# Performance work log

Measured on AMD Instinct MI355X. Metric: run time of the kernel, lower is better.

## Reference

```python
import jax, jax.numpy as jnp
import numpy as np

H, B, T, C = 1024, 256, 256, 10

def setup_inputs() -> dict:
    key = jax.random.key(0)
    ks = jax.random.split(key, 10)
    def xav(k, shape):
        fan_in, fan_out = shape[1], shape[0]
        lim = jnp.sqrt(6.0 / (fan_in + fan_out))
        return jax.random.uniform(k, shape, jnp.float32, -lim, lim)
    return {
        "x": jax.random.normal(ks[0], (B, T), jnp.float32),
        "W_gx": xav(ks[1], (H, 1)), "W_gh": xav(ks[2], (H, H)),
        "W_ix": xav(ks[3], (H, 1)), "W_ih": xav(ks[4], (H, H)),
        "W_fx": xav(ks[5], (H, 1)), "W_fh": xav(ks[6], (H, H)),
        "W_ox": xav(ks[7], (H, 1)), "W_oh": xav(ks[8], (H, H)),
        "W_ph": xav(ks[9], (C, H)),
        "b_g": jnp.zeros((B,), jnp.float32), "b_i": jnp.zeros((B,), jnp.float32),
        "b_f": jnp.zeros((B,), jnp.float32), "b_o": jnp.zeros((B,), jnp.float32),
        "b_p": jnp.zeros((B,), jnp.float32),
    }

def reference(x, W_gx, W_gh, W_ix, W_ih, W_fx, W_fh, W_ox, W_oh, W_ph,
              b_g, b_i, b_f, b_o, b_p):
    batch = x.shape[0]
    hidden = W_gh.shape[0]
    xs = x.T  # [T, B]; per-step x_t is a [1, B] row (input_dim = 1)

    def step(carry, x_t):
        h, c = carry                       # [H, B] each
        xr = x_t[None, :]                  # [1, B]
        g = jnp.tanh(W_gx @ xr + W_gh @ h + b_g)          # [H, B] + [B] broadcasts per column
        i = jax.nn.sigmoid(W_ix @ xr + W_ih @ h + b_i)
        f = jax.nn.sigmoid(W_fx @ xr + W_fh @ h + b_f)
        o = jax.nn.sigmoid(W_ox @ xr + W_oh @ h + b_o)
        c_new = g * i + c * f
        h_new = jnp.tanh(c_new) * o
        return (h_new, c_new), None

    h0 = jnp.zeros((hidden, batch), x.dtype)
    c0 = jnp.zeros((hidden, batch), x.dtype)
    (h_T, _), _ = jax.lax.scan(step, (h0, c0), xs)
    p = W_ph @ h_T + b_p                   # [C, B]
    y = jax.nn.softmax(p, axis=1)          # faithful: softmax over dim=1 (batch axis)
    return y.T                             # [B, C]
```

## Files before the change

### kernel.cpp

```cpp
#include <hip/hip_runtime.h>
#include <hip/hip_bf16.h>


#define H 1024
#define B 256
#define T 256
#define NCLS 10

typedef __attribute__((ext_vector_type(8))) short short8;
typedef __attribute__((ext_vector_type(4))) float f32x4;

__device__ inline unsigned short bf16_bits(float f) {
    union { __hip_bfloat16 h; unsigned short u; } cv;
    cv.h = __float2bfloat16(f);
    return cv.u;
}

#define L2E 1.4426950408889634f
__device__ inline float sigm_fast(float x) {
    float e = __builtin_amdgcn_exp2f(-L2E * x);
    return __builtin_amdgcn_rcpf(1.0f + e);
}
__device__ inline float tanh_fast(float x) {
    float e = __builtin_amdgcn_exp2f((2.0f * L2E) * x);
    return 1.0f - 2.0f * __builtin_amdgcn_rcpf(1.0f + e);
}


__global__ __launch_bounds__(512)
__attribute__((amdgpu_waves_per_eu(2, 2)))
void lstm_persist(
    const float* __restrict__ x,
    const float* __restrict__ Wgh, const float* __restrict__ Wih,
    const float* __restrict__ Wfh, const float* __restrict__ Woh,
    const float* __restrict__ Wgx, const float* __restrict__ Wix,
    const float* __restrict__ Wfx, const float* __restrict__ Wox,
    const float* __restrict__ bg, const float* __restrict__ bi,
    const float* __restrict__ bf_, const float* __restrict__ bo,
    char* __restrict__ frag,
    unsigned* __restrict__ flags,
    unsigned* __restrict__ det,
    float* __restrict__ hfin)
{
    __shared__ __align__(16) char hstage[65536];
    __shared__ float zb[2][4][32][36];
    __shared__ float wxl[4][32];
    __shared__ float bsl[4][32];
    __shared__ int sh_lcl;

    const int tid  = threadIdx.x;
    const int lane = tid & 63;
    const int wave = tid >> 6;
    const int gate = wave & 3;
    const int kh   = wave >> 2;
    const int bt = blockIdx.x & 7;
    const int jt = blockIdx.x >> 3;
    const int j0 = jt * 32;
    const int b0 = bt * 32;

    unsigned xcc;
    __asm__ volatile("s_getreg_b32 %0, hwreg(HW_REG_XCC_ID)" : "=s"(xcc));
    xcc &= 7u;
    if (tid == 0)
        __hip_atomic_store(&det[bt * 32 + jt], xcc + 1u,
                           __ATOMIC_RELAXED, __HIP_MEMORY_SCOPE_AGENT);

    if (tid < 128) {
        int g = tid >> 5, r = tid & 31;
        const float* wx = (g == 0) ? Wgx : (g == 1) ? Wix : (g == 2) ? Wfx : Wox;
        const float* bb = (g == 0) ? bg  : (g == 1) ? bi  : (g == 2) ? bf_ : bo;
        wxl[g][r] = wx[j0 + r];
        bsl[g][r] = bb[b0 + r];
    }

    const float* Wh = (gate == 0) ? Wgh : (gate == 1) ? Wih : (gate == 2) ? Wfh : Woh;
    short8 awreg[2][16];
#pragma unroll
    for (int mt = 0; mt < 2; ++mt) {
        const float* wrow = Wh + (j0 + 16 * mt + (lane & 15)) * H
                          + kh * 512 + ((lane >> 4) * 8);
#pragma unroll
        for (int c = 0; c < 16; ++c) {
            const float4 f0 = *(const float4*)(wrow + c * 32);
            const float4 f1 = *(const float4*)(wrow + c * 32 + 4);
            short8 s;
            s[0] = (short)bf16_bits(f0.x); s[1] = (short)bf16_bits(f0.y);
            s[2] = (short)bf16_bits(f0.z); s[3] = (short)bf16_bits(f0.w);
            s[4] = (short)bf16_bits(f1.x); s[5] = (short)bf16_bits(f1.y);
            s[6] = (short)bf16_bits(f1.z); s[7] = (short)bf16_bits(f1.w);
            awreg[mt][c] = s;
        }
    }
#pragma unroll
    for (int mt = 0; mt < 2; ++mt)
#pragma unroll
        for (int c = 0; c < 16; ++c)
            __asm__ volatile("" : "+a"(awreg[mt][c]));

    if (wave == 0) {
        unsigned v;
        while (true) {
            v = __hip_atomic_load(&det[bt * 32 + (lane & 31)],
                                  __ATOMIC_RELAXED, __HIP_MEMORY_SCOPE_AGENT);
            if (__all((int)(v != 0u))) break;
            __builtin_amdgcn_s_sleep(1);
        }
        int same = __all((int)(v == xcc + 1u));
        if (tid == 0) sh_lcl = same;
    }
    __syncthreads();
    const bool lcl = (sh_lcl != 0);

    float creg[2] = {0.f, 0.f};
    const int nn = tid & 31;
    const int aa = tid >> 5;

    unsigned* myflag = &flags[blockIdx.x * 32];
    unsigned* pollflag = &flags[(((unsigned)lane & 31) * 8 + bt) * 32];

    for (int t = 0; t < T; ++t) {
        const float xv = x[(b0 + nn) * T + t];

        if (wave == 0) {
            const unsigned target = (unsigned)t;
            while (true) {
                unsigned v = __hip_atomic_load(pollflag, __ATOMIC_RELAXED,
                                               __HIP_MEMORY_SCOPE_AGENT);
                if (__all((int)(v >= target))) break;
                __builtin_amdgcn_s_sleep(1);
            }
        }
        __syncthreads();

        f32x4 a00 = {0.f,0.f,0.f,0.f}, a01 = a00, a10 = a00, a11 = a00;

        if (t > 0) {
            {
                const char* gbase = frag + (t & 1) * 524288 + bt * 65536 + tid * 16;
                short8 v0, v1, v2, v3, v4, v5, v6, v7;
                if (lcl) {
                    __asm__ volatile(
                        "global_load_dwordx4 %0, %8, off sc0\n\t"
                        "global_load_dwordx4 %1, %9, off sc0\n\t"
                        "global_load_dwordx4 %2, %10, off sc0\n\t"
                        "global_load_dwordx4 %3, %11, off sc0\n\t"
                        "global_load_dwordx4 %4, %12, off sc0\n\t"
                        "global_load_dwordx4 %5, %13, off sc0\n\t"
                        "global_load_dwordx4 %6, %14, off sc0\n\t"
                        "global_load_dwordx4 %7, %15, off sc0\n\t"
                        "s_waitcnt vmcnt(0)"
                        : "=&v"(v0), "=&v"(v1), "=&v"(v2), "=&v"(v3),
                          "=&v"(v4), "=&v"(v5), "=&v"(v6), "=&v"(v7)
                        : "v"(gbase),         "v"(gbase + 8192),
                          "v"(gbase + 16384), "v"(gbase + 24576),
                          "v"(gbase + 32768), "v"(gbase + 40960),
                          "v"(gbase + 49152), "v"(gbase + 57344)
                        : "memory");
                } else {
                    __asm__ volatile(
                        "global_load_dwordx4 %0, %8, off sc0 sc1\n\t"
                        "global_load_dwordx4 %1, %9, off sc0 sc1\n\t"
                        "global_load_dwordx4 %2, %10, off sc0 sc1\n\t"
                        "global_load_dwordx4 %3, %11, off sc0 sc1\n\t"
                        "global_load_dwordx4 %4, %12, off sc0 sc1\n\t"
                        "global_load_dwordx4 %5, %13, off sc0 sc1\n\t"
                        "global_load_dwordx4 %6, %14, off sc0 sc1\n\t"
                        "global_load_dwordx4 %7, %15, off sc0 sc1\n\t"
                        "s_waitcnt vmcnt(0)"
                        : "=&v"(v0), "=&v"(v1), "=&v"(v2), "=&v"(v3),
                          "=&v"(v4), "=&v"(v5), "=&v"(v6), "=&v"(v7)
                        : "v"(gbase),         "v"(gbase + 8192),
                          "v"(gbase + 16384), "v"(gbase + 24576),
                          "v"(gbase + 32768), "v"(gbase + 40960),
                          "v"(gbase + 49152), "v"(gbase + 57344)
                        : "memory");
                }
                short8* dd = (short8*)hstage;
                dd[tid +    0] = v0;  dd[tid +  512] = v1;
                dd[tid + 1024] = v2;  dd[tid + 1536] = v3;
                dd[tid + 2048] = v4;  dd[tid + 2560] = v5;
                dd[tid + 3072] = v6;  dd[tid + 3584] = v7;
            }
            __syncthreads();

#pragma unroll
            for (int c = 0; c < 16; ++c) {
                const int cg = kh * 16 + c;
                short8 bf0 = *(const short8*)(hstage + cg * 1024 + lane * 16);
                short8 bf1 = *(const short8*)(hstage + 32768 + cg * 1024 + lane * 16);
                a00 = __builtin_amdgcn_mfma_f32_16x16x32_bf16(awreg[0][c], bf0, a00, 0, 0, 0);
                a01 = __builtin_amdgcn_mfma_f32_16x16x32_bf16(awreg[0][c], bf1, a01, 0, 0, 0);
                a10 = __builtin_amdgcn_mfma_f32_16x16x32_bf16(awreg[1][c], bf0, a10, 0, 0, 0);
                a11 = __builtin_amdgcn_mfma_f32_16x16x32_bf16(awreg[1][c], bf1, a11, 0, 0, 0);
            }
        }

        {
            const int cn = lane & 15;
            const int rb = (lane >> 4) * 4;
#pragma unroll
            for (int r = 0; r < 4; ++r) {
                zb[kh][gate][ 0 + rb + r][ 0 + cn] = a00[r];
                zb[kh][gate][ 0 + rb + r][16 + cn] = a01[r];
                zb[kh][gate][16 + rb + r][ 0 + cn] = a10[r];
                zb[kh][gate][16 + rb + r][16 + cn] = a11[r];
            }
        }
        __syncthreads();

        unsigned short hb[2];
#pragma unroll
        for (int q = 0; q < 2; ++q) {
            const int jl = 2 * aa + q;
            float zg = (zb[0][0][jl][nn] + zb[1][0][jl][nn]) + wxl[0][jl] * xv + bsl[0][nn];
            float zi = (zb[0][1][jl][nn] + zb[1][1][jl][nn]) + wxl[1][jl] * xv + bsl[1][nn];
            float zf = (zb[0][2][jl][nn] + zb[1][2][jl][nn]) + wxl[2][jl] * xv + bsl[2][nn];
            float zo = (zb[0][3][jl][nn] + zb[1][3][jl][nn]) + wxl[3][jl] * xv + bsl[3][nn];
            float g  = tanh_fast(zg);
            float ig = sigm_fast(zi);
            float fg = sigm_fast(zf);
            float og = sigm_fast(zo);
            creg[q] = g * ig + creg[q] * fg;
            float hn = tanh_fast(creg[q]) * og;
            hb[q] = bf16_bits(hn);
            if (t == T - 1) hfin[(j0 + jl) * B + (b0 + nn)] = hn;
        }
        {
            const unsigned val = (unsigned)hb[0] | ((unsigned)hb[1] << 16);
            short* fb = (short*)(frag + ((t + 1) & 1) * 524288);
            short* fdst = fb + ((2 * bt + (nn >> 4)) * 32 + jt) * 512
                        + ((aa >> 2) * 16 + (nn & 15)) * 8 + (aa & 3) * 2;
            if (lcl) {
                *(volatile unsigned*)fdst = val;
            } else {
                __hip_atomic_store((unsigned*)fdst, val, __ATOMIC_RELAXED,
                                   __HIP_MEMORY_SCOPE_AGENT);
            }
        }

        __syncthreads();
        if (tid == 0) {
            __asm__ volatile("s_waitcnt vmcnt(0)" ::: "memory");
            __hip_atomic_store(myflag, (unsigned)(t + 1), __ATOMIC_RELAXED,
                               __HIP_MEMORY_SCOPE_AGENT);
        }
    }
}

__global__ __launch_bounds__(256) void lstm_final(
    const float* __restrict__ Wph, const float* __restrict__ hfin,
    const float* __restrict__ bp, float* __restrict__ out)
{
    __shared__ float sh[256];
    __shared__ float shm, shs;
    int c = blockIdx.x;
    int b = threadIdx.x;
    float acc = bp[b];
    const float* wr = Wph + c * H;
    for (int k = 0; k < H; ++k)
        acc += wr[k] * hfin[k * B + b];

    sh[b] = acc;
    __syncthreads();
    for (int s = 128; s > 0; s >>= 1) {
        if (b < s) sh[b] = fmaxf(sh[b], sh[b + s]);
        __syncthreads();
    }
    if (b == 0) shm = sh[0];
    __syncthreads();
    float e = expf(acc - shm);
    sh[b] = e;
    __syncthreads();
    for (int s = 128; s > 0; s >>= 1) {
        if (b < s) sh[b] += sh[b + s];
        __syncthreads();
    }
    if (b == 0) shs = sh[0];
    __syncthreads();
    out[b * NCLS + c] = e / shs;
}

extern "C" void kernel_launch(void* const* d_in, const int* in_sizes, int n_in,
                              void* d_out, int out_size, void* d_ws, size_t ws_size,
                              hipStream_t stream)
{
    const float* x   = (const float*)d_in[0];
    const float* Wgx = (const float*)d_in[1];
    const float* Wgh = (const float*)d_in[2];
    const float* Wix = (const float*)d_in[3];
    const float* Wih = (const float*)d_in[4];
    const float* Wfx = (const float*)d_in[5];
    const float* Wfh = (const float*)d_in[6];
    const float* Wox = (const float*)d_in[7];
    const float* Woh = (const float*)d_in[8];
    const float* Wph = (const float*)d_in[9];
    const float* bg  = (const float*)d_in[10];
    const float* bi  = (const float*)d_in[11];
    const float* bfv = (const float*)d_in[12];
    const float* bo  = (const float*)d_in[13];
    const float* bp  = (const float*)d_in[14];

    char* ws = (char*)d_ws;
    char* frag = ws;
    unsigned* flags = (unsigned*)(ws + 1048576);
    unsigned* det   = (unsigned*)(ws + 1081344);
    float* hfin = (float*)(ws + 1085440);

    hipMemsetAsync(flags, 0, 36864, stream);

    lstm_persist<<<256, 512, 0, stream>>>(
        x, Wgh, Wih, Wfh, Woh, Wgx, Wix, Wfx, Wox,
        bg, bi, bfv, bo, frag, flags, det, hfin);

    lstm_final<<<NCLS, 256, 0, stream>>>(Wph, hfin, bp, (float*)d_out);
}
```

Before: 1.163 ms.

## Switch recurrent matmul to 32x32x16 MFMA with K split across four waves

Each wave now computes two gates over a 32x32 tile with 32x32x16 bf16 MFMAs, and the K dimension is split into quarters across four waves instead of halves. Partial sums are written to a swizzled LDS buffer and reduced by 256 threads, which each produce four hidden rows and store 64-bit packed bf16 fragments in a new layout. The aim is fewer MFMA issues and fewer B-fragment LDS reads per step. In exchange the LDS reduction grows to four partials, and half the threads sit idle during the elementwise phase.

```diff
diff --git a/kernel.cpp b/kernel.cpp
--- a/kernel.cpp
+++ b/kernel.cpp
@@ -9,6 +9,8 @@
 
 typedef __attribute__((ext_vector_type(8))) short short8;
 typedef __attribute__((ext_vector_type(4))) float f32x4;
+typedef __attribute__((ext_vector_type(16))) float f32x16;
+typedef unsigned long long ull;
 
 __device__ inline unsigned short bf16_bits(float f) {
     union { __hip_bfloat16 h; unsigned short u; } cv;
@@ -43,7 +45,7 @@
     float* __restrict__ hfin)
 {
     __shared__ __align__(16) char hstage[65536];
-    __shared__ float zb[2][4][32][36];
+    __shared__ __align__(16) float zb[16][32][32];
     __shared__ float wxl[4][32];
     __shared__ float bsl[4][32];
     __shared__ int sh_lcl;
@@ -51,8 +53,8 @@
     const int tid  = threadIdx.x;
     const int lane = tid & 63;
     const int wave = tid >> 6;
-    const int gate = wave & 3;
-    const int kh   = wave >> 2;
+    const int gp   = wave >> 2;
+    const int kq   = wave & 3;
     const int bt = blockIdx.x & 7;
     const int jt = blockIdx.x >> 3;
     const int j0 = jt * 32;
@@ -73,29 +75,31 @@
         bsl[g][r] = bb[b0 + r];
     }
 
-    const float* Wh = (gate == 0) ? Wgh : (gate == 1) ? Wih : (gate == 2) ? Wfh : Woh;
+    const float* Wlo = (gp == 0) ? Wgh : Wfh;
+    const float* Whi = (gp == 0) ? Wih : Woh;
     short8 awreg[2][16];
 #pragma unroll
-    for (int mt = 0; mt < 2; ++mt) {
-        const float* wrow = Wh + (j0 + 16 * mt + (lane & 15)) * H
-                          + kh * 512 + ((lane >> 4) * 8);
+    for (int gg = 0; gg < 2; ++gg) {
+        const float* Wp = gg ? Whi : Wlo;
+        const float* wrow = Wp + (j0 + (lane & 31)) * H
+                          + kq * 256 + ((lane >> 5) * 8);
 #pragma unroll
         for (int c = 0; c < 16; ++c) {
-            const float4 f0 = *(const float4*)(wrow + c * 32);
-            const float4 f1 = *(const float4*)(wrow + c * 32 + 4);
+            const float4 f0 = *(const float4*)(wrow + c * 16);
+            const float4 f1 = *(const float4*)(wrow + c * 16 + 4);
             short8 s;
             s[0] = (short)bf16_bits(f0.x); s[1] = (short)bf16_bits(f0.y);
             s[2] = (short)bf16_bits(f0.z); s[3] = (short)bf16_bits(f0.w);
             s[4] = (short)bf16_bits(f1.x); s[5] = (short)bf16_bits(f1.y);
             s[6] = (short)bf16_bits(f1.z); s[7] = (short)bf16_bits(f1.w);
-            awreg[mt][c] = s;
-        }
-    }
-#pragma unroll
-    for (int mt = 0; mt < 2; ++mt)
+            awreg[gg][c] = s;
+        }
+    }
+#pragma unroll
+    for (int gg = 0; gg < 2; ++gg)
 #pragma unroll
         for (int c = 0; c < 16; ++c)
-            __asm__ volatile("" : "+a"(awreg[mt][c]));
+            __asm__ volatile("" : "+a"(awreg[gg][c]));
 
     if (wave == 0) {
         unsigned v;
@@ -111,7 +115,7 @@
     __syncthreads();
     const bool lcl = (sh_lcl != 0);
 
-    float creg[2] = {0.f, 0.f};
+    float creg[4] = {0.f, 0.f, 0.f, 0.f};
     const int nn = tid & 31;
     const int aa = tid >> 5;
 
@@ -132,7 +136,9 @@
         }
         __syncthreads();
 
-        f32x4 a00 = {0.f,0.f,0.f,0.f}, a01 = a00, a10 = a00, a11 = a00;
+        f32x16 acc0 = {0.f,0.f,0.f,0.f,0.f,0.f,0.f,0.f,
+                       0.f,0.f,0.f,0.f,0.f,0.f,0.f,0.f};
+        f32x16 acc1 = acc0;
 
         if (t > 0) {
             {
@@ -185,55 +191,73 @@
 
 #pragma unroll
             for (int c = 0; c < 16; ++c) {
-                const int cg = kh * 16 + c;
-                short8 bf0 = *(const short8*)(hstage + cg * 1024 + lane * 16);
-                short8 bf1 = *(const short8*)(hstage + 32768 + cg * 1024 + lane * 16);
-                a00 = __builtin_amdgcn_mfma_f32_16x16x32_bf16(awreg[0][c], bf0, a00, 0, 0, 0);
-                a01 = __builtin_amdgcn_mfma_f32_16x16x32_bf16(awreg[0][c], bf1, a01, 0, 0, 0);
-                a10 = __builtin_amdgcn_mfma_f32_16x16x32_bf16(awreg[1][c], bf0, a10, 0, 0, 0);
-                a11 = __builtin_amdgcn_mfma_f32_16x16x32_bf16(awreg[1][c], bf1, a11, 0, 0, 0);
+                const int ks = (kq << 4) + c;
+                short8 bf = *(const short8*)(hstage + ks * 1024 + lane * 16);
+                acc0 = __builtin_amdgcn_mfma_f32_32x32x16_bf16(awreg[0][c], bf, acc0, 0, 0, 0);
+                acc1 = __builtin_amdgcn_mfma_f32_32x32x16_bf16(awreg[1][c], bf, acc1, 0, 0, 0);
             }
         }
 
         {
-            const int cn = lane & 15;
-            const int rb = (lane >> 4) * 4;
-#pragma unroll
-            for (int r = 0; r < 4; ++r) {
-                zb[kh][gate][ 0 + rb + r][ 0 + cn] = a00[r];
-                zb[kh][gate][ 0 + rb + r][16 + cn] = a01[r];
-                zb[kh][gate][16 + rb + r][ 0 + cn] = a10[r];
-                zb[kh][gate][16 + rb + r][16 + cn] = a11[r];
-            }
-        }
-        __syncthreads();
-
-        unsigned short hb[2];
-#pragma unroll
-        for (int q = 0; q < 2; ++q) {
-            const int jl = 2 * aa + q;
-            float zg = (zb[0][0][jl][nn] + zb[1][0][jl][nn]) + wxl[0][jl] * xv + bsl[0][nn];
-            float zi = (zb[0][1][jl][nn] + zb[1][1][jl][nn]) + wxl[1][jl] * xv + bsl[1][nn];
-            float zf = (zb[0][2][jl][nn] + zb[1][2][jl][nn]) + wxl[2][jl] * xv + bsl[2][nn];
-            float zo = (zb[0][3][jl][nn] + zb[1][3][jl][nn]) + wxl[3][jl] * xv + bsl[3][nn];
-            float g  = tanh_fast(zg);
-            float ig = sigm_fast(zi);
-            float fg = sigm_fast(zf);
-            float og = sigm_fast(zo);
-            creg[q] = g * ig + creg[q] * fg;
-            float hn = tanh_fast(creg[q]) * og;
-            hb[q] = bf16_bits(hn);
-            if (t == T - 1) hfin[(j0 + jl) * B + (b0 + nn)] = hn;
-        }
-        {
-            const unsigned val = (unsigned)hb[0] | ((unsigned)hb[1] << 16);
-            short* fb = (short*)(frag + ((t + 1) & 1) * 524288);
-            short* fdst = fb + ((2 * bt + (nn >> 4)) * 32 + jt) * 512
-                        + ((aa >> 2) * 16 + (nn & 15)) * 8 + (aa & 3) * 2;
+            float* zbF = &zb[0][0][0];
+            const int col = lane & 31;
+            const int hi  = lane >> 5;
+            const int g0 = gp * 2, g1 = g0 + 1;
+#pragma unroll
+            for (int rq = 0; rq < 4; ++rq) {
+                const int sw = ((2 * rq + hi) ^ (col & 7)) << 2;
+                f32x4 w0, w1;
+#pragma unroll
+                for (int e = 0; e < 4; ++e) {
+                    w0[e] = acc0[rq * 4 + e];
+                    w1[e] = acc1[rq * 4 + e];
+                }
+                *(f32x4*)(zbF + ((kq * 4 + g0) << 10) + (col << 5) + sw) = w0;
+                *(f32x4*)(zbF + ((kq * 4 + g1) << 10) + (col << 5) + sw) = w1;
+            }
+        }
+        __syncthreads();
+
+        if (tid < 256) {
+            const int r0 = aa * 4;
+            const float* zbF = &zb[0][0][0];
+            const int sw = (aa ^ (nn & 7)) << 2;
+            f32x4 zs[4];
+#pragma unroll
+            for (int gi = 0; gi < 4; ++gi) {
+                f32x4 s = *(const f32x4*)(zbF + (gi << 10) + (nn << 5) + sw);
+#pragma unroll
+                for (int kk = 1; kk < 4; ++kk)
+                    s += *(const f32x4*)(zbF + (((kk << 2) + gi) << 10) + (nn << 5) + sw);
+                zs[gi] = s;
+            }
+            unsigned short hb[4];
+#pragma unroll
+            for (int q = 0; q < 4; ++q) {
+                const int row = r0 + q;
+                float zg = zs[0][q] + wxl[0][row] * xv + bsl[0][nn];
+                float zi = zs[1][q] + wxl[1][row] * xv + bsl[1][nn];
+                float zf = zs[2][q] + wxl[2][row] * xv + bsl[2][nn];
+                float zo = zs[3][q] + wxl[3][row] * xv + bsl[3][nn];
+                float g  = tanh_fast(zg);
+                float ig = sigm_fast(zi);
+                float fg = sigm_fast(zf);
+                float og = sigm_fast(zo);
+                creg[q] = g * ig + creg[q] * fg;
+                float hn = tanh_fast(creg[q]) * og;
+                hb[q] = bf16_bits(hn);
+                if (t == T - 1) hfin[(j0 + row) * B + (b0 + nn)] = hn;
+            }
+            const ull val = (ull)hb[0] | ((ull)hb[1] << 16)
+                          | ((ull)hb[2] << 32) | ((ull)hb[3] << 48);
+            const int jp = j0 + r0;
+            short* fb = (short*)(frag + ((t + 1) & 1) * 524288) + bt * 32768;
+            short* fdst = fb + (jp >> 4) * 512 + ((jp >> 3) & 1) * 256
+                        + nn * 8 + (jp & 7);
             if (lcl) {
-                *(volatile unsigned*)fdst = val;
+                *(volatile ull*)fdst = val;
             } else {
-                __hip_atomic_store((unsigned*)fdst, val, __ATOMIC_RELAXED,
+                __hip_atomic_store((ull*)fdst, val, __ATOMIC_RELAXED,
                                    __HIP_MEMORY_SCOPE_AGENT);
             }
         }
```

New measurement: 1.211 ms. 1.04x slower.
